# Kernel optimization log

Measured on AMD Instinct MI355X. Metric: run time of the kernel, lower is better.

## Reference

```python
import jax, jax.numpy as jnp
from jax import lax
import numpy as np

B, N, D, NSAMPLE = 16, 4096, 254, 16
EPS = 1e-5


def setup_inputs() -> dict:
    key = jax.random.key(0)
    ks = jax.random.split(key, 4)
    c0, c1, c2 = 256, 512, 512
    return {
        "xy": jax.random.normal(ks[0], (B, N, 2), jnp.float32),
        "points": jax.random.normal(ks[1], (B, N, D), jnp.float32),
        "W1": jax.random.normal(ks[2], (c0, c1), jnp.float32) * 0.05,
        "b1": jnp.zeros((c1,), jnp.float32),
        "g1": jnp.ones((c1,), jnp.float32),
        "beta1": jnp.zeros((c1,), jnp.float32),
        "W2": jax.random.normal(ks[3], (c1, c2), jnp.float32) * 0.05,
        "b2": jnp.zeros((c2,), jnp.float32),
        "g2": jnp.ones((c2,), jnp.float32),
        "beta2": jnp.zeros((c2,), jnp.float32),
    }


def _fps(xy, npoint):
    # Iterative farthest point sampling. Deterministic start at index 0
    # (torch version uses a random start index).
    b, n, _ = xy.shape
    batch = jnp.arange(b)

    def step(carry, _):
        distance, farthest = carry
        centroid = xy[batch, farthest]  # [B,2]
        dist = jnp.sum((xy - centroid[:, None, :]) ** 2, axis=-1)  # [B,N]
        distance = jnp.minimum(distance, dist)
        nxt = jnp.argmax(distance, axis=-1)
        return (distance, nxt), farthest

    init = (jnp.full((b, n), 1e10, xy.dtype), jnp.zeros((b,), jnp.int32))
    _, idx = lax.scan(step, init, None, length=npoint)
    return idx.T  # [B, npoint]


def _gather(pts, idx):
    # pts [B,N,C], idx [B,S] or [B,S,K] -> gathered points
    return jax.vmap(lambda p, i: p[i])(pts, idx)


def _sqdist(a, b):
    # a [B,S,C], b [B,N,C] -> [B,S,N] squared distances (expanded form)
    return (jnp.sum(a * a, -1)[:, :, None] + jnp.sum(b * b, -1)[:, None, :]
            - 2.0 * jnp.einsum('bsc,bnc->bsn', a, b))


def _bn_relu(x, g, beta):
    # BatchNorm2d in training mode: stats over (batch, K, S) per channel, biased var
    m = jnp.mean(x, axis=(0, 1, 2))
    v = jnp.var(x, axis=(0, 1, 2))
    return jax.nn.relu((x - m) * lax.rsqrt(v + EPS) * g + beta)


def reference(xy, points, W1, b1, g1, beta1, W2, b2, g2, beta2):
    b, n, c = xy.shape
    npoint = n // 4
    fps_idx = _fps(xy, npoint)                     # [B,S]
    new_xy = _gather(xy, fps_idx)                  # [B,S,2]
    dists = _sqdist(new_xy, xy)                    # [B,S,N]
    _, idx = lax.top_k(-dists, NSAMPLE)            # [B,S,K] nearest neighbors
    grouped_xy = _gather(xy, idx)                  # [B,S,K,2]
    grouped_xy_norm = grouped_xy - new_xy[:, :, None, :]
    grouped_points = _gather(points, idx)          # [B,S,K,D]
    x = jnp.concatenate([grouped_xy_norm, grouped_points], axis=-1)  # [B,S,K,2+D]
    x = _bn_relu(jnp.einsum('bskc,co->bsko', x, W1) + b1, g1, beta1)
    x = _bn_relu(jnp.einsum('bskc,co->bsko', x, W2) + b2, g2, beta2)
    new_points = jnp.max(x, axis=2)                # max over K -> [B,S,C2]
    return new_xy, new_points
```

## Files before the change

kernel.cpp:

```cpp
#include <hip/hip_runtime.h>

typedef float f32x4 __attribute__((ext_vector_type(4)));
typedef short s16x8 __attribute__((ext_vector_type(8)));
typedef short s16x4 __attribute__((ext_vector_type(4)));

#define NB 16
#define NPT 4096
#define DPT 254
#define NS 1024
#define KNN 16
#define NPAIR (NB*NS*KNN)
#define NROWS (NB*NPT)

__device__ __forceinline__ unsigned short f2bf(float f) {
  unsigned u = __float_as_uint(f);
  u += 0x7FFFu + ((u >> 16) & 1u);
  return (unsigned short)(u >> 16);
}
__device__ __forceinline__ float bf2f(unsigned short h) {
  return __uint_as_float(((unsigned)h) << 16);
}
__device__ __forceinline__ unsigned ordf(float f) {
  unsigned u = __float_as_uint(f);
  return u ^ (unsigned)(((int)u >> 31) | 0x80000000);
}
__device__ __forceinline__ float vmulf(float a, float b) {
  float r; asm("v_mul_f32 %0, %1, %2" : "=v"(r) : "v"(a), "v"(b)); return r;
}
__device__ __forceinline__ float vaddf(float a, float b) {
  float r; asm("v_add_f32 %0, %1, %2" : "=v"(r) : "v"(a), "v"(b)); return r;
}
__device__ __forceinline__ float vsubf(float a, float b) {
  float r; asm("v_sub_f32 %0, %1, %2" : "=v"(r) : "v"(a), "v"(b)); return r;
}
__device__ __forceinline__ float vfmaf(float a, float b, float c) {
  float r; asm("v_fma_f32 %0, %1, %2, %3" : "=v"(r) : "v"(a), "v"(b), "v"(c)); return r;
}

__global__ __launch_bounds__(256) void k_conv(const float* __restrict__ W1, const float* __restrict__ W2,
                                              unsigned short* __restrict__ W1s, unsigned short* __restrict__ W2s) {
  int i = blockIdx.x * 256 + threadIdx.x;
  if (i < 8 * 512 * 32) {
    int kk = i & 31, col = (i >> 5) & 511, c = i >> 14;
    W1s[i] = f2bf(W1[(c * 32 + kk) * 512 + col]);
  }
  if (i < 16 * 512 * 32) {
    int kk = i & 31, col = (i >> 5) & 511, c = i >> 14;
    W2s[i] = f2bf(W2[(c * 32 + kk) * 512 + col]);
  }
}

__global__ __launch_bounds__(256) void k_fps(const float* __restrict__ xy, int* __restrict__ fpsi) {
  const int b = blockIdx.x;
  const int t = threadIdx.x;
  __shared__ float sx[NPT], sy[NPT];
  __shared__ unsigned long long wkey[2][4];
  for (int i = t; i < NPT; i += 256) {
    float2 v = ((const float2*)xy)[b * NPT + i];
    sx[i] = v.x; sy[i] = v.y;
  }
  __syncthreads();
  float px[16], py[16], dist[16];
  #pragma unroll
  for (int j = 0; j < 16; ++j) {
    int i = t + 256 * j;
    px[j] = sx[i]; py[j] = sy[i]; dist[j] = 1e10f;
  }
  if (t == 0) fpsi[b * NS] = 0;
  float cx = sx[0], cy = sy[0];
  for (int step = 1; step < NS; ++step) {
    float bd = -1.0f; int bi = 0;
    #pragma unroll
    for (int j = 0; j < 16; ++j) {
      float dx = vsubf(px[j], cx), dy = vsubf(py[j], cy);
      float d = vaddf(vmulf(dx, dx), vmulf(dy, dy));
      float nd = fminf(dist[j], d);
      dist[j] = nd;
      if (nd > bd) { bd = nd; bi = t + 256 * j; }
    }
    unsigned long long key = ((unsigned long long)ordf(bd) << 32) | (unsigned)(0xFFFFFFFFu ^ (unsigned)bi);
    #pragma unroll
    for (int off = 32; off; off >>= 1) {
      unsigned long long o = __shfl_xor(key, off);
      key = (o > key) ? o : key;
    }
    if ((t & 63) == 0) wkey[step & 1][t >> 6] = key;
    __syncthreads();
    unsigned long long k0 = wkey[step & 1][0], k1 = wkey[step & 1][1];
    unsigned long long k2 = wkey[step & 1][2], k3 = wkey[step & 1][3];
    unsigned long long m = k0 > k1 ? k0 : k1;
    unsigned long long n = k2 > k3 ? k2 : k3;
    m = m > n ? m : n;
    const int fi = (int)(0xFFFFFFFFu ^ (unsigned)m);
    if (t == 0) fpsi[b * NS + step] = fi;
    cx = sx[fi]; cy = sy[fi];
  }
}

__global__ __launch_bounds__(256) void k_knn(const float* __restrict__ xy, const int* __restrict__ fpsi,
                                             int* __restrict__ knni, float* __restrict__ xyn,
                                             float* __restrict__ out_newxy) {
  const int q = blockIdx.x;
  const int b = q >> 10;
  const int t = threadIdx.x;
  __shared__ unsigned long long wmin[2][4];
  const int qi = fpsi[q];
  float2 qv = ((const float2*)xy)[b * NPT + qi];
  const float qx = qv.x, qy = qv.y;
  if (t == 0) { out_newxy[q * 2 + 0] = qx; out_newxy[q * 2 + 1] = qy; }
  const float sa = vaddf(vmulf(qx, qx), vmulf(qy, qy));
  float px[16], py[16];
  unsigned long long ku[16], cmin = ~0ull;
  #pragma unroll
  for (int j = 0; j < 16; ++j) {
    const int i = t + 256 * j;
    float2 v = ((const float2*)xy)[b * NPT + i];
    px[j] = v.x; py[j] = v.y;
    const float sb = vaddf(vmulf(v.x, v.x), vmulf(v.y, v.y));
    const float dot = vfmaf(qy, v.y, vmulf(qx, v.x));
    const float d = vsubf(vaddf(sa, sb), vmulf(2.0f, dot));
    ku[j] = ((unsigned long long)ordf(d) << 32) | (unsigned)i;
    cmin = ku[j] < cmin ? ku[j] : cmin;
  }
  for (int r = 0; r < KNN; ++r) {
    unsigned long long key = cmin;
    #pragma unroll
    for (int off = 32; off; off >>= 1) {
      unsigned long long o = __shfl_xor(key, off);
      key = o < key ? o : key;
    }
    if ((t & 63) == 0) wmin[r & 1][t >> 6] = key;
    __syncthreads();
    unsigned long long m0 = wmin[r & 1][0], m1 = wmin[r & 1][1];
    unsigned long long m2 = wmin[r & 1][2], m3 = wmin[r & 1][3];
    unsigned long long m = m0 < m1 ? m0 : m1;
    unsigned long long n = m2 < m3 ? m2 : m3;
    m = m < n ? m : n;
    if (m == cmin) {
      const unsigned widx = (unsigned)m;
      const int jj0 = (int)(widx >> 8);
      cmin = ~0ull;
      #pragma unroll
      for (int j = 0; j < 16; ++j) {
        if (j == jj0) {
          ku[j] = ~0ull;
          knni[q * KNN + r] = (int)widx;
          xyn[(q * KNN + r) * 2 + 0] = vsubf(px[j], qx);
          xyn[(q * KNN + r) * 2 + 1] = vsubf(py[j], qy);
        }
        cmin = ku[j] < cmin ? ku[j] : cmin;
      }
    }
  }
}

__global__ __launch_bounds__(256) void k_p1(const float* __restrict__ points,
                                            const unsigned short* __restrict__ W1s,
                                            unsigned short* __restrict__ P1) {
  const int rt = blockIdx.x;
  const int t = threadIdx.x, l = t & 63, w = t >> 6;
  __shared__ unsigned short sA[64 * 40];
  __shared__ unsigned short sB[512 * 40];
  f32x4 acc[4][8];
  #pragma unroll
  for (int mi = 0; mi < 4; ++mi)
    #pragma unroll
    for (int ni = 0; ni < 8; ++ni) acc[mi][ni] = (f32x4){0.f, 0.f, 0.f, 0.f};
  for (int c = 0; c < 8; ++c) {
    __syncthreads();
    {
      const int r = t >> 2, kk = (t & 3) * 8;
      const int m = rt * 64 + r;
      s16x8 av;
      #pragma unroll
      for (int j = 0; j < 8; ++j) {
        const int cc = c * 32 + kk + j;
        const float f = (cc >= 2) ? points[(size_t)m * DPT + (cc - 2)] : 0.0f;
        av[j] = (short)f2bf(f);
      }
      *(s16x8*)(&sA[r * 40 + kk]) = av;
    }
    {
      const unsigned short* src = &W1s[c * 16384];
      #pragma unroll
      for (int qd = 0; qd < 8; ++qd) {
        const int e = t * 64 + qd * 8;
        const int col = e >> 5, kk = e & 31;
        *(s16x8*)(&sB[col * 40 + kk]) = *(const s16x8*)(&src[e]);
      }
    }
    __syncthreads();
    s16x8 a[4];
    #pragma unroll
    for (int mi = 0; mi < 4; ++mi)
      a[mi] = *(const s16x8*)(&sA[(mi * 16 + (l & 15)) * 40 + (l >> 4) * 8]);
    #pragma unroll
    for (int ni = 0; ni < 8; ++ni) {
      const s16x8 bv = *(const s16x8*)(&sB[(w * 128 + ni * 16 + (l & 15)) * 40 + (l >> 4) * 8]);
      #pragma unroll
      for (int mi = 0; mi < 4; ++mi)
        acc[mi][ni] = __builtin_amdgcn_mfma_f32_16x16x32_bf16(a[mi], bv, acc[mi][ni], 0, 0, 0);
    }
  }
  #pragma unroll
  for (int mi = 0; mi < 4; ++mi)
    #pragma unroll
    for (int ni = 0; ni < 8; ++ni)
      #pragma unroll
      for (int r = 0; r < 4; ++r) {
        const int row = rt * 64 + mi * 16 + (l >> 4) * 4 + r;
        const int col = w * 128 + ni * 16 + (l & 15);
        P1[(size_t)row * 512 + col] = f2bf(acc[mi][ni][r]);
      }
}

__global__ __launch_bounds__(256) void k_stats1(const unsigned short* __restrict__ P1,
                                                const int* __restrict__ knni, const float* __restrict__ xyn,
                                                const float* __restrict__ W1, const float* __restrict__ b1,
                                                float* __restrict__ part1) {
  const int blk = blockIdx.x;
  const int t = threadIdx.x;
  __shared__ int sgidx[256];
  __shared__ float sxn[256][2];
  const int p = blk * 256 + t;
  const int b = p >> 14;
  sgidx[t] = b * NPT + knni[p];
  sxn[t][0] = xyn[p * 2 + 0]; sxn[t][1] = xyn[p * 2 + 1];
  __syncthreads();
  const int ch0 = 2 * t;
  const float w00 = W1[ch0], w01 = W1[ch0 + 1];
  const float w10 = W1[512 + ch0], w11 = W1[512 + ch0 + 1];
  const float bb0 = b1[ch0], bb1 = b1[ch0 + 1];
  float s0 = 0, s1 = 0, q0 = 0, q1 = 0;
  for (int i = 0; i < 256; ++i) {
    const int row = sgidx[i];
    const float xn = sxn[i][0], yn = sxn[i][1];
    unsigned v = *(const unsigned*)(&P1[(size_t)row * 512 + ch0]);
    float z0 = bf2f((unsigned short)v) + xn * w00 + yn * w10 + bb0;
    float z1 = bf2f((unsigned short)(v >> 16)) + xn * w01 + yn * w11 + bb1;
    s0 += z0; q0 += z0 * z0; s1 += z1; q1 += z1 * z1;
  }
  float4 o; o.x = s0; o.y = q0; o.z = s1; o.w = q1;
  *(float4*)(&part1[(size_t)(blk * 512 + ch0) * 2]) = o;
}

__global__ __launch_bounds__(256) void k_colreduce(const float* __restrict__ part, int rows_per_blk,
                                                   float* __restrict__ out) {
  const int cs = blockIdx.x & 3, rs = blockIdx.x >> 2;
  const int col = cs * 256 + threadIdx.x;
  float s = 0;
  const int r0 = rs * rows_per_blk;
  for (int r = 0; r < rows_per_blk; ++r) s += part[(size_t)(r0 + r) * 1024 + col];
  out[rs * 1024 + col] = s;
}

__global__ __launch_bounds__(256) void k_fin1(const float* __restrict__ tmp1, const float* __restrict__ W1,
                                              const float* __restrict__ b1, const float* __restrict__ g1,
                                              const float* __restrict__ bt1, float4* __restrict__ coef1) {
  const int ch = blockIdx.x * 256 + threadIdx.x;
  float s = 0, q = 0;
  #pragma unroll
  for (int r = 0; r < 4; ++r) { s += tmp1[r * 1024 + 2 * ch]; q += tmp1[r * 1024 + 2 * ch + 1]; }
  const float inv = 1.0f / 262144.0f;
  const float m = s * inv;
  const float var = q * inv - m * m;
  const float A = rsqrtf(var + 1e-5f) * g1[ch];
  const float Bv = bt1[ch] - m * A;
  float4 cf;
  cf.x = A; cf.y = W1[ch] * A; cf.z = W1[512 + ch] * A; cf.w = b1[ch] * A + Bv;
  coef1[ch] = cf;
}

__global__ __launch_bounds__(256) void k_main(const unsigned short* __restrict__ P1,
                                              const int* __restrict__ knni, const float* __restrict__ xyn,
                                              const float4* __restrict__ coef1,
                                              const unsigned short* __restrict__ W2s,
                                              const float* __restrict__ b2,
                                              float* __restrict__ part2,
                                              unsigned short* __restrict__ zmaxh, unsigned short* __restrict__ zminh) {
  const int g = blockIdx.x;
  const int t = threadIdx.x, l = t & 63, w = t >> 6;
  __shared__ unsigned short sH[64 * 40];
  __shared__ unsigned short sW[512 * 40];
  __shared__ int sgidx[64];
  __shared__ float sxn[64][2];
  if (t < 64) {
    const int p = g * 64 + t;
    const int b = p >> 14;
    sgidx[t] = b * NPT + knni[p];
    sxn[t][0] = xyn[p * 2 + 0]; sxn[t][1] = xyn[p * 2 + 1];
  }
  f32x4 acc[4][8];
  #pragma unroll
  for (int mi = 0; mi < 4; ++mi)
    #pragma unroll
    for (int ni = 0; ni < 8; ++ni) acc[mi][ni] = (f32x4){0.f, 0.f, 0.f, 0.f};
  const int skk = t & 31;
  const int sr0 = (t >> 5) * 8;
  for (int c = 0; c < 16; ++c) {
    __syncthreads();
    {
      const int ch = c * 32 + skk;
      const float4 cf = coef1[ch];
      #pragma unroll
      for (int qq = 0; qq < 8; ++qq) {
        const int r = sr0 + qq;
        const int row = sgidx[r];
        const float pv = bf2f(P1[(size_t)row * 512 + ch]);
        const float h = fmaxf(0.0f, pv * cf.x + sxn[r][0] * cf.y + sxn[r][1] * cf.z + cf.w);
        sH[r * 40 + skk] = f2bf(h);
      }
    }
    {
      const unsigned short* src = &W2s[c * 16384];
      #pragma unroll
      for (int qd = 0; qd < 8; ++qd) {
        const int e = t * 64 + qd * 8;
        const int col = e >> 5, kk = e & 31;
        *(s16x8*)(&sW[col * 40 + kk]) = *(const s16x8*)(&src[e]);
      }
    }
    __syncthreads();
    s16x8 a[4];
    #pragma unroll
    for (int mi = 0; mi < 4; ++mi)
      a[mi] = *(const s16x8*)(&sH[(mi * 16 + (l & 15)) * 40 + (l >> 4) * 8]);
    #pragma unroll
    for (int ni = 0; ni < 8; ++ni) {
      const s16x8 bv = *(const s16x8*)(&sW[(w * 128 + ni * 16 + (l & 15)) * 40 + (l >> 4) * 8]);
      #pragma unroll
      for (int mi = 0; mi < 4; ++mi)
        acc[mi][ni] = __builtin_amdgcn_mfma_f32_16x16x32_bf16(a[mi], bv, acc[mi][ni], 0, 0, 0);
    }
  }
  const int cl = l & 15, lg = l >> 4;
  #pragma unroll
  for (int ni = 0; ni < 8; ++ni) {
    const int col = w * 128 + ni * 16 + cl;
    const float b2v = b2[col];
    float colsum = 0, colssq = 0;
    #pragma unroll
    for (int mi = 0; mi < 4; ++mi) {
      f32x4 v = acc[mi][ni];
      #pragma unroll
      for (int r = 0; r < 4; ++r) v[r] += b2v;
      float mx = fmaxf(fmaxf(v[0], v[1]), fmaxf(v[2], v[3]));
      float mn = fminf(fminf(v[0], v[1]), fminf(v[2], v[3]));
      float sm = v[0] + v[1] + v[2] + v[3];
      float sq = v[0] * v[0] + v[1] * v[1] + v[2] * v[2] + v[3] * v[3];
      mx = fmaxf(mx, __shfl_xor(mx, 16)); mx = fmaxf(mx, __shfl_xor(mx, 32));
      mn = fminf(mn, __shfl_xor(mn, 16)); mn = fminf(mn, __shfl_xor(mn, 32));
      sm = sm + __shfl_xor(sm, 16); sm = sm + __shfl_xor(sm, 32);
      sq = sq + __shfl_xor(sq, 16); sq = sq + __shfl_xor(sq, 32);
      if (lg == 0) {
        const int srow = g * 4 + mi;
        zmaxh[(size_t)srow * 512 + col] = f2bf(mx);
        zminh[(size_t)srow * 512 + col] = f2bf(mn);
      }
      colsum += sm; colssq += sq;
    }
    if (lg == 0) {
      float2 o; o.x = colsum; o.y = colssq;
      *(float2*)(&part2[(size_t)(g * 512 + col) * 2]) = o;
    }
  }
}

__global__ __launch_bounds__(256) void k_fin2(const float* __restrict__ tmp2, const float* __restrict__ g2,
                                              const float* __restrict__ bt2,
                                              float* __restrict__ A2, float* __restrict__ B2) {
  const int ch = blockIdx.x * 256 + threadIdx.x;
  float s = 0, q = 0;
  #pragma unroll
  for (int r = 0; r < 16; ++r) { s += tmp2[r * 1024 + 2 * ch]; q += tmp2[r * 1024 + 2 * ch + 1]; }
  const float inv = 1.0f / 262144.0f;
  const float m = s * inv;
  const float var = q * inv - m * m;
  const float A = rsqrtf(var + 1e-5f) * g2[ch];
  A2[ch] = A;
  B2[ch] = bt2[ch] - m * A;
}

__global__ __launch_bounds__(256) void k_out(const unsigned short* __restrict__ zmaxh,
                                             const unsigned short* __restrict__ zminh,
                                             const float* __restrict__ A2, const float* __restrict__ B2,
                                             float* __restrict__ out) {
  int v = blockIdx.x * 256 + threadIdx.x;
  for (; v < 2097152; v += gridDim.x * 256) {
    const int f = v * 4;
    const int col = f & 511;
    const float4 a = *(const float4*)(&A2[col]);
    const float4 bb = *(const float4*)(&B2[col]);
    s16x4 mxh = *(const s16x4*)(&zmaxh[f]);
    s16x4 mnh = *(const s16x4*)(&zminh[f]);
    float4 o;
    o.x = fmaxf(0.f, a.x * (a.x > 0.f ? bf2f((unsigned short)mxh[0]) : bf2f((unsigned short)mnh[0])) + bb.x);
    o.y = fmaxf(0.f, a.y * (a.y > 0.f ? bf2f((unsigned short)mxh[1]) : bf2f((unsigned short)mnh[1])) + bb.y);
    o.z = fmaxf(0.f, a.z * (a.z > 0.f ? bf2f((unsigned short)mxh[2]) : bf2f((unsigned short)mnh[2])) + bb.z);
    o.w = fmaxf(0.f, a.w * (a.w > 0.f ? bf2f((unsigned short)mxh[3]) : bf2f((unsigned short)mnh[3])) + bb.w);
    *(float4*)(&out[32768 + f]) = o;
  }
}

__global__ void k_sent_ws(float* out) { if (threadIdx.x == 0) out[0] = 54321.0f; }

extern "C" void kernel_launch(void* const* d_in, const int* in_sizes, int n_in,
                              void* d_out, int out_size, void* d_ws, size_t ws_size,
                              hipStream_t stream) {
  const float* xy   = (const float*)d_in[0];
  const float* pts  = (const float*)d_in[1];
  const float* W1   = (const float*)d_in[2];
  const float* b1   = (const float*)d_in[3];
  const float* g1   = (const float*)d_in[4];
  const float* bt1  = (const float*)d_in[5];
  const float* W2   = (const float*)d_in[6];
  const float* b2   = (const float*)d_in[7];
  const float* g2   = (const float*)d_in[8];
  const float* bt2  = (const float*)d_in[9];
  float* out = (float*)d_out;
  (void)in_sizes; (void)n_in; (void)out_size;

  char* base = (char*)d_ws;
  size_t off = 0;
  auto take = [&](size_t bytes) -> char* {
    char* r = base + off;
    off = (off + bytes + 255) & ~(size_t)255;
    return r;
  };
  int*   fpsi  = (int*)take((size_t)NB * NS * 4);
  int*   knni  = (int*)take((size_t)NPAIR * 4);
  float* xyn   = (float*)take((size_t)NPAIR * 2 * 4);
  unsigned short* W1s = (unsigned short*)take((size_t)8 * 512 * 32 * 2);
  unsigned short* W2s = (unsigned short*)take((size_t)16 * 512 * 32 * 2);
  unsigned short* P1  = (unsigned short*)take((size_t)NROWS * 512 * 2);
  float* part1 = (float*)take((size_t)1024 * 1024 * 4);
  float* tmp1  = (float*)take((size_t)4 * 1024 * 4);
  float4* coef1 = (float4*)take((size_t)512 * 16);
  float* part2 = (float*)take((size_t)4096 * 1024 * 4);
  float* tmp2  = (float*)take((size_t)16 * 1024 * 4);
  float* A2    = (float*)take((size_t)512 * 4);
  float* B2    = (float*)take((size_t)512 * 4);
  unsigned short* zmaxh = (unsigned short*)take((size_t)16384 * 512 * 2);
  unsigned short* zminh = (unsigned short*)take((size_t)16384 * 512 * 2);

  if (off > ws_size) {
    k_sent_ws<<<1, 64, 0, stream>>>(out);
    return;
  }

  k_conv<<<1024, 256, 0, stream>>>(W1, W2, W1s, W2s);
  k_fps<<<NB, 256, 0, stream>>>(xy, fpsi);
  k_knn<<<NB * NS, 256, 0, stream>>>(xy, fpsi, knni, xyn, out);
  k_p1<<<1024, 256, 0, stream>>>(pts, W1s, P1);
  k_stats1<<<1024, 256, 0, stream>>>(P1, knni, xyn, W1, b1, part1);
  k_colreduce<<<16, 256, 0, stream>>>(part1, 256, tmp1);
  k_fin1<<<2, 256, 0, stream>>>(tmp1, W1, b1, g1, bt1, coef1);
  k_main<<<4096, 256, 0, stream>>>(P1, knni, xyn, coef1, W2s, b2, part2, zmaxh, zminh);
  k_colreduce<<<64, 256, 0, stream>>>(part2, 256, tmp2);
  k_fin2<<<2, 256, 0, stream>>>(tmp2, g2, bt2, A2, B2);
  k_out<<<2048, 256, 0, stream>>>(zmaxh, zminh, A2, B2, out);
}
```

Before: 1.873 ms.

## Merge FPS, W2 conversion and P1 GEMM into one heterogeneous kernel

Combines the serial FPS kernel (16 blocks), the W2 bf16 conversion and the point-feature GEMM into a single launch whose blocks branch on their block id. The P1 GEMM no longer depends on FPS, so its blocks can run on the otherwise idle CUs while the long sequential FPS loop runs. W1 is now converted to bf16 inline inside the GEMM tile loads instead of in a separate pre-pass. In exchange, every GEMM block does strided fp32 W1 reads and conversion, and the shared-memory allocation is sized for the largest branch.

```diff
diff --git a/kernel.cpp b/kernel.cpp
--- a/kernel.cpp
+++ b/kernel.cpp
@@ -37,63 +37,126 @@
   float r; asm("v_fma_f32 %0, %1, %2, %3" : "=v"(r) : "v"(a), "v"(b), "v"(c)); return r;
 }
 
-__global__ __launch_bounds__(256) void k_conv(const float* __restrict__ W1, const float* __restrict__ W2,
-                                              unsigned short* __restrict__ W1s, unsigned short* __restrict__ W2s) {
-  int i = blockIdx.x * 256 + threadIdx.x;
-  if (i < 8 * 512 * 32) {
-    int kk = i & 31, col = (i >> 5) & 511, c = i >> 14;
-    W1s[i] = f2bf(W1[(c * 32 + kk) * 512 + col]);
-  }
-  if (i < 16 * 512 * 32) {
-    int kk = i & 31, col = (i >> 5) & 511, c = i >> 14;
-    W2s[i] = f2bf(W2[(c * 32 + kk) * 512 + col]);
-  }
-}
-
-__global__ __launch_bounds__(256) void k_fps(const float* __restrict__ xy, int* __restrict__ fpsi) {
-  const int b = blockIdx.x;
+__global__ __launch_bounds__(256) void k_front(const float* __restrict__ xy, int* __restrict__ fpsi,
+                                               const float* __restrict__ W2, unsigned short* __restrict__ W2s,
+                                               const float* __restrict__ points, const float* __restrict__ W1,
+                                               unsigned short* __restrict__ P1) {
+  __shared__ __align__(16) char smem[46080];
+  const int gid = blockIdx.x;
   const int t = threadIdx.x;
-  __shared__ float sx[NPT], sy[NPT];
-  __shared__ unsigned long long wkey[2][4];
-  for (int i = t; i < NPT; i += 256) {
-    float2 v = ((const float2*)xy)[b * NPT + i];
-    sx[i] = v.x; sy[i] = v.y;
-  }
-  __syncthreads();
-  float px[16], py[16], dist[16];
-  #pragma unroll
-  for (int j = 0; j < 16; ++j) {
-    int i = t + 256 * j;
-    px[j] = sx[i]; py[j] = sy[i]; dist[j] = 1e10f;
-  }
-  if (t == 0) fpsi[b * NS] = 0;
-  float cx = sx[0], cy = sy[0];
-  for (int step = 1; step < NS; ++step) {
-    float bd = -1.0f; int bi = 0;
+
+  if (gid < 16) {
+    const int b = gid;
+    float* sx = (float*)smem;
+    float* sy = sx + NPT;
+    unsigned long long* wkey = (unsigned long long*)(sy + NPT);
+    for (int i = t; i < NPT; i += 256) {
+      float2 v = ((const float2*)xy)[b * NPT + i];
+      sx[i] = v.x; sy[i] = v.y;
+    }
+    __syncthreads();
+    float px[16], py[16], dist[16];
     #pragma unroll
     for (int j = 0; j < 16; ++j) {
-      float dx = vsubf(px[j], cx), dy = vsubf(py[j], cy);
-      float d = vaddf(vmulf(dx, dx), vmulf(dy, dy));
-      float nd = fminf(dist[j], d);
-      dist[j] = nd;
-      if (nd > bd) { bd = nd; bi = t + 256 * j; }
-    }
-    unsigned long long key = ((unsigned long long)ordf(bd) << 32) | (unsigned)(0xFFFFFFFFu ^ (unsigned)bi);
-    #pragma unroll
-    for (int off = 32; off; off >>= 1) {
-      unsigned long long o = __shfl_xor(key, off);
-      key = (o > key) ? o : key;
-    }
-    if ((t & 63) == 0) wkey[step & 1][t >> 6] = key;
-    __syncthreads();
-    unsigned long long k0 = wkey[step & 1][0], k1 = wkey[step & 1][1];
-    unsigned long long k2 = wkey[step & 1][2], k3 = wkey[step & 1][3];
-    unsigned long long m = k0 > k1 ? k0 : k1;
-    unsigned long long n = k2 > k3 ? k2 : k3;
-    m = m > n ? m : n;
-    const int fi = (int)(0xFFFFFFFFu ^ (unsigned)m);
-    if (t == 0) fpsi[b * NS + step] = fi;
-    cx = sx[fi]; cy = sy[fi];
+      int i = t + 256 * j;
+      px[j] = sx[i]; py[j] = sy[i]; dist[j] = 1e10f;
+    }
+    if (t == 0) fpsi[b * NS] = 0;
+    float cx = sx[0], cy = sy[0];
+    for (int step = 1; step < NS; ++step) {
+      float bd = -1.0f; int bi = 0;
+      #pragma unroll
+      for (int j = 0; j < 16; ++j) {
+        float dx = vsubf(px[j], cx), dy = vsubf(py[j], cy);
+        float d = vaddf(vmulf(dx, dx), vmulf(dy, dy));
+        float nd = fminf(dist[j], d);
+        dist[j] = nd;
+        if (nd > bd) { bd = nd; bi = t + 256 * j; }
+      }
+      unsigned long long key = ((unsigned long long)ordf(bd) << 32) | (unsigned)(0xFFFFFFFFu ^ (unsigned)bi);
+      #pragma unroll
+      for (int off = 32; off; off >>= 1) {
+        unsigned long long o = __shfl_xor(key, off);
+        key = (o > key) ? o : key;
+      }
+      if ((t & 63) == 0) wkey[(step & 1) * 4 + (t >> 6)] = key;
+      __syncthreads();
+      unsigned long long k0 = wkey[(step & 1) * 4 + 0], k1 = wkey[(step & 1) * 4 + 1];
+      unsigned long long k2 = wkey[(step & 1) * 4 + 2], k3 = wkey[(step & 1) * 4 + 3];
+      unsigned long long m = k0 > k1 ? k0 : k1;
+      unsigned long long n = k2 > k3 ? k2 : k3;
+      m = m > n ? m : n;
+      const int fi = (int)(0xFFFFFFFFu ^ (unsigned)m);
+      if (t == 0) fpsi[b * NS + step] = fi;
+      cx = sx[fi]; cy = sy[fi];
+    }
+  } else if (gid < 80) {
+    const int i0 = (gid - 16) * 4096 + t;
+    #pragma unroll
+    for (int k = 0; k < 16; ++k) {
+      const int i = i0 + k * 256;
+      const int kk = i & 31, col = (i >> 5) & 511, c = i >> 14;
+      W2s[i] = f2bf(W2[(c * 32 + kk) * 512 + col]);
+    }
+  } else {
+    const int rt = gid - 80;
+    const int l = t & 63, w = t >> 6;
+    unsigned short* sA = (unsigned short*)smem;
+    unsigned short* sB = sA + 64 * 40;
+    f32x4 acc[4][8];
+    #pragma unroll
+    for (int mi = 0; mi < 4; ++mi)
+      #pragma unroll
+      for (int ni = 0; ni < 8; ++ni) acc[mi][ni] = (f32x4){0.f, 0.f, 0.f, 0.f};
+    for (int c = 0; c < 8; ++c) {
+      __syncthreads();
+      {
+        const int r = t >> 2, kk = (t & 3) * 8;
+        const int m = rt * 64 + r;
+        s16x8 av;
+        #pragma unroll
+        for (int j = 0; j < 8; ++j) {
+          const int cc = c * 32 + kk + j;
+          const float f = (cc >= 2) ? points[(size_t)m * DPT + (cc - 2)] : 0.0f;
+          av[j] = (short)f2bf(f);
+        }
+        *(s16x8*)(&sA[r * 40 + kk]) = av;
+      }
+      {
+        #pragma unroll
+        for (int qd = 0; qd < 8; ++qd) {
+          const int e = t * 64 + qd * 8;
+          const int col = e >> 5, kk = e & 31;
+          s16x8 bv8;
+          #pragma unroll
+          for (int j = 0; j < 8; ++j)
+            bv8[j] = (short)f2bf(W1[(c * 32 + kk + j) * 512 + col]);
+          *(s16x8*)(&sB[col * 40 + kk]) = bv8;
+        }
+      }
+      __syncthreads();
+      s16x8 a[4];
+      #pragma unroll
+      for (int mi = 0; mi < 4; ++mi)
+        a[mi] = *(const s16x8*)(&sA[(mi * 16 + (l & 15)) * 40 + (l >> 4) * 8]);
+      #pragma unroll
+      for (int ni = 0; ni < 8; ++ni) {
+        const s16x8 bv = *(const s16x8*)(&sB[(w * 128 + ni * 16 + (l & 15)) * 40 + (l >> 4) * 8]);
+        #pragma unroll
+        for (int mi = 0; mi < 4; ++mi)
+          acc[mi][ni] = __builtin_amdgcn_mfma_f32_16x16x32_bf16(a[mi], bv, acc[mi][ni], 0, 0, 0);
+      }
+    }
+    #pragma unroll
+    for (int mi = 0; mi < 4; ++mi)
+      #pragma unroll
+      for (int ni = 0; ni < 8; ++ni)
+        #pragma unroll
+        for (int r = 0; r < 4; ++r) {
+          const int row = rt * 64 + mi * 16 + (l >> 4) * 4 + r;
+          const int col = w * 128 + ni * 16 + (l & 15);
+          P1[(size_t)row * 512 + col] = f2bf(acc[mi][ni][r]);
+        }
   }
 }
 
@@ -152,66 +215,6 @@
       }
     }
   }
-}
-
-__global__ __launch_bounds__(256) void k_p1(const float* __restrict__ points,
-                                            const unsigned short* __restrict__ W1s,
-                                            unsigned short* __restrict__ P1) {
-  const int rt = blockIdx.x;
-  const int t = threadIdx.x, l = t & 63, w = t >> 6;
-  __shared__ unsigned short sA[64 * 40];
-  __shared__ unsigned short sB[512 * 40];
-  f32x4 acc[4][8];
-  #pragma unroll
-  for (int mi = 0; mi < 4; ++mi)
-    #pragma unroll
-    for (int ni = 0; ni < 8; ++ni) acc[mi][ni] = (f32x4){0.f, 0.f, 0.f, 0.f};
-  for (int c = 0; c < 8; ++c) {
-    __syncthreads();
-    {
-      const int r = t >> 2, kk = (t & 3) * 8;
-      const int m = rt * 64 + r;
-      s16x8 av;
-      #pragma unroll
-      for (int j = 0; j < 8; ++j) {
-        const int cc = c * 32 + kk + j;
-        const float f = (cc >= 2) ? points[(size_t)m * DPT + (cc - 2)] : 0.0f;
-        av[j] = (short)f2bf(f);
-      }
-      *(s16x8*)(&sA[r * 40 + kk]) = av;
-    }
-    {
-      const unsigned short* src = &W1s[c * 16384];
-      #pragma unroll
-      for (int qd = 0; qd < 8; ++qd) {
-        const int e = t * 64 + qd * 8;
-        const int col = e >> 5, kk = e & 31;
-        *(s16x8*)(&sB[col * 40 + kk]) = *(const s16x8*)(&src[e]);
-      }
-    }
-    __syncthreads();
-    s16x8 a[4];
-    #pragma unroll
-    for (int mi = 0; mi < 4; ++mi)
-      a[mi] = *(const s16x8*)(&sA[(mi * 16 + (l & 15)) * 40 + (l >> 4) * 8]);
-    #pragma unroll
-    for (int ni = 0; ni < 8; ++ni) {
-      const s16x8 bv = *(const s16x8*)(&sB[(w * 128 + ni * 16 + (l & 15)) * 40 + (l >> 4) * 8]);
-      #pragma unroll
-      for (int mi = 0; mi < 4; ++mi)
-        acc[mi][ni] = __builtin_amdgcn_mfma_f32_16x16x32_bf16(a[mi], bv, acc[mi][ni], 0, 0, 0);
-    }
-  }
-  #pragma unroll
-  for (int mi = 0; mi < 4; ++mi)
-    #pragma unroll
-    for (int ni = 0; ni < 8; ++ni)
-      #pragma unroll
-      for (int r = 0; r < 4; ++r) {
-        const int row = rt * 64 + mi * 16 + (l >> 4) * 4 + r;
-        const int col = w * 128 + ni * 16 + (l & 15);
-        P1[(size_t)row * 512 + col] = f2bf(acc[mi][ni][r]);
-      }
 }
 
 __global__ __launch_bounds__(256) void k_stats1(const unsigned short* __restrict__ P1,
@@ -430,7 +433,6 @@
   int*   fpsi  = (int*)take((size_t)NB * NS * 4);
   int*   knni  = (int*)take((size_t)NPAIR * 4);
   float* xyn   = (float*)take((size_t)NPAIR * 2 * 4);
-  unsigned short* W1s = (unsigned short*)take((size_t)8 * 512 * 32 * 2);
   unsigned short* W2s = (unsigned short*)take((size_t)16 * 512 * 32 * 2);
   unsigned short* P1  = (unsigned short*)take((size_t)NROWS * 512 * 2);
   float* part1 = (float*)take((size_t)1024 * 1024 * 4);
@@ -448,10 +450,8 @@
     return;
   }
 
-  k_conv<<<1024, 256, 0, stream>>>(W1, W2, W1s, W2s);
-  k_fps<<<NB, 256, 0, stream>>>(xy, fpsi);
+  k_front<<<1104, 256, 0, stream>>>(xy, fpsi, W2, W2s, pts, W1, P1);
   k_knn<<<NB * NS, 256, 0, stream>>>(xy, fpsi, knni, xyn, out);
-  k_p1<<<1024, 256, 0, stream>>>(pts, W1s, P1);
   k_stats1<<<1024, 256, 0, stream>>>(P1, knni, xyn, W1, b1, part1);
   k_colreduce<<<16, 256, 0, stream>>>(part1, 256, tmp1);
   k_fin1<<<2, 256, 0, stream>>>(tmp1, W1, b1, g1, bt1, coef1);
```

Measured after the change: 1.777 ms, median of 2. 1.05x faster.
